# Kernel tuning notes

Hardware: AMD Instinct MI355X
Metric: run time of the kernel (lower is better)

## Reference

```python
import jax, jax.numpy as jnp
import numpy as np

WP, WF, OUT_W = 10, 10, 110  # past/future window, fixed alpha width from source


def setup_inputs() -> dict:
    key = jax.random.key(0)
    k1, k2, k3 = jax.random.split(key, 3)
    B, L, D = 4096, 110, 200
    node_features = jax.random.normal(k1, (B, L, D), dtype=jnp.float32)
    text_len_tensor = jax.random.randint(k2, (B,), 1, L + 1)  # valid lengths in [1, L]
    var = 2.0 / (D + D)  # init std from source
    weight = jax.random.normal(k3, (D, D), dtype=jnp.float32) * var
    return {"node_features": node_features, "text_len_tensor": text_len_tensor, "weight": weight}


def reference(node_features, text_len_tensor, weight):
    B, L, D = node_features.shape
    # att_matrix[b,k] = W @ x[b,k]
    att = jnp.einsum('de,bke->bkd', weight, node_features)
    # score[b,j,k] = att[b,k] . x[b,j]  (query token j attends over window of k)
    scores = jnp.einsum('bkd,bjd->bjk', att, node_features)
    j = jnp.arange(L)[None, :, None]
    k = jnp.arange(L)[None, None, :]
    lens = text_len_tensor[:, None, None]
    s = jnp.maximum(j - WP, 0)
    e = jnp.minimum(j + WF, lens - 1)
    mask = (k >= s) & (k <= e) & (j < lens)
    probs = jax.nn.softmax(jnp.where(mask, scores, jnp.asarray(-1e9, scores.dtype)), axis=-1)
    probs = jnp.where(mask, probs, jnp.asarray(0.0, probs.dtype))
    # scatter into fixed-width alpha [L, 110] per batch, rows j>=len stay zero
    out = jnp.zeros((B, L, OUT_W), node_features.dtype).at[:, :, :L].set(probs)
    return out
```

## Files before the change

kernel.cpp:

```cpp
#include <hip/hip_runtime.h>
#include <stdint.h>

typedef short short8 __attribute__((ext_vector_type(8)));
typedef float floatx4 __attribute__((ext_vector_type(4)));
typedef int int4v __attribute__((ext_vector_type(4)));

#define NB 4096
#define LL 110
#define DD 200
#define WPP 10
#define WFF 10
#define OUTW 110

#define MTI 7
#define NTI 13
#define KCH 7
#define LDSTR 232

static __device__ __forceinline__ short f32_bf16_rn(float f) {
    uint32_t u = __float_as_uint(f);
    u += 0x7FFFu + ((u >> 16) & 1u);
    return (short)(u >> 16);
}

__global__ void EdgeAtt_wswz(const float* __restrict__ W, short* __restrict__ wswz) {
    const int nt = blockIdx.x / KCH;
    const int kc = blockIdx.x % KCH;
    const int l  = threadIdx.x;
    const int e  = nt * 16 + (l & 15);
    const int db = kc * 32 + (l >> 4) * 8;
    short8 v;
#pragma unroll
    for (int i = 0; i < 8; ++i) {
        int d = db + i;
        float x = (d < DD && e < DD) ? W[d * DD + e] : 0.0f;
        v[i] = f32_bf16_rn(x);
    }
    *(short8*)(wswz + ((size_t)(kc * NTI + nt) * 64 + l) * 8) = v;
}

__global__ __launch_bounds__(512) void EdgeAtt_fused(
    const float* __restrict__ nf, const int* __restrict__ lens,
    const short* __restrict__ wswz, float* __restrict__ out)
{
    __shared__ short nfb[112 * LDSTR];
    __shared__ short ylds[112 * LDSTR];
    const int b    = blockIdx.x;
    const int tid  = threadIdx.x;
    const int lane = tid & 63;
    const int wave = tid >> 6;
    const int len  = lens[b];

    {
        int4v z = {0, 0, 0, 0};
        for (int i = tid; i < (112 * LDSTR) / 8; i += 512) {
            ((int4v*)nfb)[i]  = z;
            ((int4v*)ylds)[i] = z;
        }
    }
    __syncthreads();

    {
        const float4* src = (const float4*)(nf + (size_t)b * LL * DD);
        for (int idx = tid; idx < (LL * DD) / 4; idx += 512) {
            float4 v = src[idx];
            int j = (idx * 4) / DD;
            int d = (idx * 4) % DD;
            uint32_t lo = ((uint32_t)(uint16_t)f32_bf16_rn(v.y) << 16) | (uint16_t)f32_bf16_rn(v.x);
            uint32_t hi = ((uint32_t)(uint16_t)f32_bf16_rn(v.w) << 16) | (uint16_t)f32_bf16_rn(v.z);
            uint32_t* dst = (uint32_t*)&nfb[j * LDSTR + d];
            dst[0] = lo;
            dst[1] = hi;
        }
    }
    __syncthreads();

    {
        const int wm   = wave >> 2;
        const int wn   = wave & 3;
        const int arow = lane & 15;
        const int acol = (lane >> 4) * 8;
        for (int nt = wn; nt < NTI; nt += 4) {
            short8 bf[KCH];
#pragma unroll
            for (int kc = 0; kc < KCH; ++kc)
                bf[kc] = *(const short8*)(wswz + ((size_t)(kc * NTI + nt) * 64 + lane) * 8);
            for (int mt = wm; mt < MTI; mt += 2) {
                floatx4 acc = {0.f, 0.f, 0.f, 0.f};
                const short* abase = &nfb[(mt * 16 + arow) * LDSTR + acol];
#pragma unroll
                for (int kc = 0; kc < KCH; ++kc) {
                    short8 a = *(const short8*)(abase + kc * 32);
                    acc = __builtin_amdgcn_mfma_f32_16x16x32_bf16(a, bf[kc], acc, 0, 0, 0);
                }
                const int col = nt * 16 + (lane & 15);
                const int rb  = mt * 16 + (lane >> 4) * 4;
#pragma unroll
                for (int i = 0; i < 4; ++i)
                    ylds[(rb + i) * LDSTR + col] = f32_bf16_rn(acc[i]);
            }
        }
    }
    __syncthreads();

    if (wave < 7) {
        const int jt = wave;
        int kts[3];
#pragma unroll
        for (int t = 0; t < 3; ++t) {
            int kt = jt - 1 + t;
            kt = kt < 0 ? 0 : kt;
            kt = kt > (MTI - 1) ? (MTI - 1) : kt;
            kts[t] = kt;
        }
        floatx4 acc[3] = {{0,0,0,0},{0,0,0,0},{0,0,0,0}};
        const int r16  = lane & 15;
        const int acol = (lane >> 4) * 8;
#pragma unroll
        for (int kc = 0; kc < KCH; ++kc) {
            short8 a = *(const short8*)&ylds[(jt * 16 + r16) * LDSTR + kc * 32 + acol];
#pragma unroll
            for (int t = 0; t < 3; ++t) {
                short8 bb = *(const short8*)&nfb[(kts[t] * 16 + r16) * LDSTR + kc * 32 + acol];
                acc[t] = __builtin_amdgcn_mfma_f32_16x16x32_bf16(a, bb, acc[t], 0, 0, 0);
            }
        }
        const int g  = lane >> 4;
        const int kl = lane & 15;
#pragma unroll
        for (int i = 0; i < 4; ++i) {
            const int j = jt * 16 + g * 4 + i;
            if (j >= LL) continue;
            const bool jv = (j < len);
            int slo = j - WPP; slo = slo < 0 ? 0 : slo;
            int shi = j + WFF; { int lm = len - 1; shi = shi > lm ? lm : shi; }
            float sv[3], ev[3];
            bool  kv[3];
            float m = -1e30f;
#pragma unroll
            for (int t = 0; t < 3; ++t) {
                int k = kts[t] * 16 + kl;
                bool tv = (t == 0) || (kts[t] != kts[t - 1]);
                kv[t] = jv && tv && (k >= slo) && (k <= shi);
                sv[t] = acc[t][i];
                if (kv[t]) m = fmaxf(m, sv[t]);
            }
#pragma unroll
            for (int o = 1; o < 16; o <<= 1) m = fmaxf(m, __shfl_xor(m, o, 64));
            float sum = 0.f;
#pragma unroll
            for (int t = 0; t < 3; ++t) {
                ev[t] = kv[t] ? __expf(sv[t] - m) : 0.f;
                sum += ev[t];
            }
#pragma unroll
            for (int o = 1; o < 16; o <<= 1) sum += __shfl_xor(sum, o, 64);
            const float inv = jv ? (1.0f / sum) : 0.0f;
            float* orow = out + ((size_t)b * LL + j) * OUTW;
#pragma unroll
            for (int kt = 0; kt < 7; ++kt) {
                int k = kt * 16 + kl;
                if (k >= OUTW) continue;
                float v = 0.0f;
                if      (kts[0] == kt) v = ev[0] * inv;
                else if (kts[1] == kt) v = ev[1] * inv;
                else if (kts[2] == kt) v = ev[2] * inv;
                orow[k] = v;
            }
        }
    }
}

extern "C" void kernel_launch(void* const* d_in, const int* in_sizes, int n_in,
                              void* d_out, int out_size, void* d_ws, size_t ws_size,
                              hipStream_t stream) {
    const float* nf   = (const float*)d_in[0];
    const int*   lens = (const int*)d_in[1];
    const float* W    = (const float*)d_in[2];
    short* wswz = (short*)d_ws;
    float* out  = (float*)d_out;

    hipLaunchKernelGGL(EdgeAtt_wswz, dim3(KCH * NTI), dim3(64), 0, stream, W, wswz);
    hipLaunchKernelGGL(EdgeAtt_fused, dim3(NB), dim3(512), 0, stream, nf, lens, wswz, out);
}
```

Baseline: 678.3 us.

## Split each batch across two blocks by query-row halves to raise occupancy

Each batch item is now handled by two blocks. Each block covers a range of query rows (0-63 or 64-109) and loads only the key rows its band window needs (80 or 64 rows). This shrinks LDS per block from two 112-row buffers so more blocks fit per CU, and launch bounds request 4 blocks. The cost is redundant loading and conversion of the overlapping rows (48-79), plus a restructured W-projection GEMM where each wave keeps its A fragments in registers and streams W from global/L2.

```diff
diff --git a/kernel.cpp b/kernel.cpp
--- a/kernel.cpp
+++ b/kernel.cpp
@@ -12,10 +12,12 @@
 #define WFF 10
 #define OUTW 110
 
-#define MTI 7
 #define NTI 13
 #define KCH 7
 #define LDSTR 232
+
+#define NFROWS 80
+#define YROWS 64
 
 static __device__ __forceinline__ short f32_bf16_rn(float f) {
     uint32_t u = __float_as_uint(f);
@@ -39,78 +41,84 @@
     *(short8*)(wswz + ((size_t)(kc * NTI + nt) * 64 + l) * 8) = v;
 }
 
-__global__ __launch_bounds__(512) void EdgeAtt_fused(
+__global__ __launch_bounds__(512, 4) void EdgeAtt_fused(
     const float* __restrict__ nf, const int* __restrict__ lens,
     const short* __restrict__ wswz, float* __restrict__ out)
 {
-    __shared__ short nfb[112 * LDSTR];
-    __shared__ short ylds[112 * LDSTR];
-    const int b    = blockIdx.x;
+    __shared__ short nfb[NFROWS * LDSTR];
+    __shared__ short ylds[YROWS * LDSTR];
+    const int b    = blockIdx.x >> 1;
+    const int h    = blockIdx.x & 1;
     const int tid  = threadIdx.x;
     const int lane = tid & 63;
     const int wave = tid >> 6;
     const int len  = lens[b];
 
+    const int base  = h ? 48 : 0;
+    const int nrows = h ? 64 : 80;
+    const int j0    = h ? 64 : 0;
+    const int njt   = h ? 3  : 4;
+
     {
         int4v z = {0, 0, 0, 0};
-        for (int i = tid; i < (112 * LDSTR) / 8; i += 512) {
-            ((int4v*)nfb)[i]  = z;
-            ((int4v*)ylds)[i] = z;
-        }
+        for (int i = tid; i < (NFROWS * LDSTR) / 8; i += 512) ((int4v*)nfb)[i] = z;
+        for (int i = tid; i < (YROWS * LDSTR) / 8; i += 512)  ((int4v*)ylds)[i] = z;
     }
     __syncthreads();
 
     {
         const float4* src = (const float4*)(nf + (size_t)b * LL * DD);
-        for (int idx = tid; idx < (LL * DD) / 4; idx += 512) {
-            float4 v = src[idx];
-            int j = (idx * 4) / DD;
-            int d = (idx * 4) % DD;
-            uint32_t lo = ((uint32_t)(uint16_t)f32_bf16_rn(v.y) << 16) | (uint16_t)f32_bf16_rn(v.x);
-            uint32_t hi = ((uint32_t)(uint16_t)f32_bf16_rn(v.w) << 16) | (uint16_t)f32_bf16_rn(v.z);
-            uint32_t* dst = (uint32_t*)&nfb[j * LDSTR + d];
-            dst[0] = lo;
-            dst[1] = hi;
-        }
-    }
-    __syncthreads();
-
-    {
-        const int wm   = wave >> 2;
-        const int wn   = wave & 3;
-        const int arow = lane & 15;
-        const int acol = (lane >> 4) * 8;
-        for (int nt = wn; nt < NTI; nt += 4) {
-            short8 bf[KCH];
-#pragma unroll
-            for (int kc = 0; kc < KCH; ++kc)
-                bf[kc] = *(const short8*)(wswz + ((size_t)(kc * NTI + nt) * 64 + lane) * 8);
-            for (int mt = wm; mt < MTI; mt += 2) {
-                floatx4 acc = {0.f, 0.f, 0.f, 0.f};
-                const short* abase = &nfb[(mt * 16 + arow) * LDSTR + acol];
-#pragma unroll
-                for (int kc = 0; kc < KCH; ++kc) {
-                    short8 a = *(const short8*)(abase + kc * 32);
-                    acc = __builtin_amdgcn_mfma_f32_16x16x32_bf16(a, bf[kc], acc, 0, 0, 0);
-                }
-                const int col = nt * 16 + (lane & 15);
-                const int rb  = mt * 16 + (lane >> 4) * 4;
-#pragma unroll
-                for (int i = 0; i < 4; ++i)
-                    ylds[(rb + i) * LDSTR + col] = f32_bf16_rn(acc[i]);
+        const int nf4 = nrows * (DD / 4);
+        for (int idx = tid; idx < nf4; idx += 512) {
+            int rl = idx / (DD / 4);
+            int d  = (idx % (DD / 4)) * 4;
+            int rg = base + rl;
+            if (rg < LL) {
+                float4 v = src[rg * (DD / 4) + d / 4];
+                uint32_t lo = ((uint32_t)(uint16_t)f32_bf16_rn(v.y) << 16) | (uint16_t)f32_bf16_rn(v.x);
+                uint32_t hi = ((uint32_t)(uint16_t)f32_bf16_rn(v.w) << 16) | (uint16_t)f32_bf16_rn(v.z);
+                uint32_t* dst = (uint32_t*)&nfb[rl * LDSTR + d];
+                dst[0] = lo;
+                dst[1] = hi;
             }
         }
     }
     __syncthreads();
 
-    if (wave < 7) {
-        const int jt = wave;
+    if (wave < 2 * njt) {
+        const int mt_l = wave % njt;
+        const int wn   = wave / njt;
+        const int rowA = (j0 - base) + mt_l * 16 + (lane & 15);
+        const int acol = (lane >> 4) * 8;
+        short8 af[KCH];
+#pragma unroll
+        for (int kc = 0; kc < KCH; ++kc)
+            af[kc] = *(const short8*)&nfb[rowA * LDSTR + kc * 32 + acol];
+        for (int nt = wn; nt < NTI; nt += 2) {
+            floatx4 acc = {0.f, 0.f, 0.f, 0.f};
+#pragma unroll
+            for (int kc = 0; kc < KCH; ++kc) {
+                short8 bf = *(const short8*)(wswz + ((size_t)(kc * NTI + nt) * 64 + lane) * 8);
+                acc = __builtin_amdgcn_mfma_f32_16x16x32_bf16(af[kc], bf, acc, 0, 0, 0);
+            }
+            const int col = nt * 16 + (lane & 15);
+            const int rb  = mt_l * 16 + (lane >> 4) * 4;
+#pragma unroll
+            for (int i = 0; i < 4; ++i)
+                ylds[(rb + i) * LDSTR + col] = f32_bf16_rn(acc[i]);
+        }
+    }
+    __syncthreads();
+
+    if (wave < njt) {
+        const int jt_g = j0 / 16 + wave;
+        const int ktb  = base / 16;
         int kts[3];
 #pragma unroll
         for (int t = 0; t < 3; ++t) {
-            int kt = jt - 1 + t;
+            int kt = jt_g - 1 + t;
             kt = kt < 0 ? 0 : kt;
-            kt = kt > (MTI - 1) ? (MTI - 1) : kt;
+            kt = kt > 6 ? 6 : kt;
             kts[t] = kt;
         }
         floatx4 acc[3] = {{0,0,0,0},{0,0,0,0},{0,0,0,0}};
@@ -118,10 +126,10 @@
         const int acol = (lane >> 4) * 8;
 #pragma unroll
         for (int kc = 0; kc < KCH; ++kc) {
-            short8 a = *(const short8*)&ylds[(jt * 16 + r16) * LDSTR + kc * 32 + acol];
+            short8 a = *(const short8*)&ylds[(wave * 16 + r16) * LDSTR + kc * 32 + acol];
 #pragma unroll
             for (int t = 0; t < 3; ++t) {
-                short8 bb = *(const short8*)&nfb[(kts[t] * 16 + r16) * LDSTR + kc * 32 + acol];
+                short8 bb = *(const short8*)&nfb[((kts[t] - ktb) * 16 + r16) * LDSTR + kc * 32 + acol];
                 acc[t] = __builtin_amdgcn_mfma_f32_16x16x32_bf16(a, bb, acc[t], 0, 0, 0);
             }
         }
@@ -129,7 +137,7 @@
         const int kl = lane & 15;
 #pragma unroll
         for (int i = 0; i < 4; ++i) {
-            const int j = jt * 16 + g * 4 + i;
+            const int j = jt_g * 16 + g * 4 + i;
             if (j >= LL) continue;
             const bool jv = (j < len);
             int slo = j - WPP; slo = slo < 0 ? 0 : slo;
@@ -181,5 +189,5 @@
     float* out  = (float*)d_out;
 
     hipLaunchKernelGGL(EdgeAtt_wswz, dim3(KCH * NTI), dim3(64), 0, stream, W, wswz);
-    hipLaunchKernelGGL(EdgeAtt_fused, dim3(NB), dim3(512), 0, stream, nf, lens, wswz, out);
+    hipLaunchKernelGGL(EdgeAtt_fused, dim3(NB * 2), dim3(512), 0, stream, nf, lens, wswz, out);
 }
```

Result: faster. 664.7 us (-2.0%).

## Restructure to one wave per 16-row query tile with register-resident intermediate

Applied to the files above, without the earlier changes.

Replaces the per-batch block with per-wave units (batch, query tile). Each wave loads its node-feature fragments straight from global memory into registers and computes the transposed W·x product with W held in LDS. It then reshuffles the bf16 accumulators across lanes to form the A operand for the score MFMA, so no intermediate goes through LDS. This removes the LDS zeroing, the staging and the block-wide barriers, and raises occupancy. In exchange, the neighbouring key tiles are re-read from global memory (L2), the 13 accumulators increase register pressure, and every block copies W into LDS.

```diff
diff --git a/kernel.cpp b/kernel.cpp
--- a/kernel.cpp
+++ b/kernel.cpp
@@ -4,6 +4,7 @@
 typedef short short8 __attribute__((ext_vector_type(8)));
 typedef float floatx4 __attribute__((ext_vector_type(4)));
 typedef int int4v __attribute__((ext_vector_type(4)));
+typedef unsigned int uint;
 
 #define NB 4096
 #define LL 110
@@ -12,15 +13,16 @@
 #define WFF 10
 #define OUTW 110
 
-#define MTI 7
 #define NTI 13
 #define KCH 7
-#define LDSTR 232
 
 static __device__ __forceinline__ short f32_bf16_rn(float f) {
     uint32_t u = __float_as_uint(f);
     u += 0x7FFFu + ((u >> 16) & 1u);
     return (short)(u >> 16);
+}
+static __device__ __forceinline__ uint pack2bf(float lo, float hi) {
+    return ((uint)(unsigned short)f32_bf16_rn(hi) << 16) | (unsigned short)f32_bf16_rn(lo);
 }
 
 __global__ void EdgeAtt_wswz(const float* __restrict__ W, short* __restrict__ wswz) {
@@ -39,134 +41,145 @@
     *(short8*)(wswz + ((size_t)(kc * NTI + nt) * 64 + l) * 8) = v;
 }
 
-__global__ __launch_bounds__(512) void EdgeAtt_fused(
+static __device__ __forceinline__ short8 ld_nf_frag(const float* __restrict__ nf,
+                                                    int b, int rt, int kc, int g, int r) {
+    short8 s = {0, 0, 0, 0, 0, 0, 0, 0};
+    const int cb = kc * 32 + g * 8;
+    if (cb < DD) {
+        int row = rt * 16 + r;
+        row = row > (LL - 1) ? (LL - 1) : row;
+        const float* p = nf + ((size_t)b * LL + row) * DD + cb;
+        float4 a = *(const float4*)p;
+        float4 c = *(const float4*)(p + 4);
+        s[0] = f32_bf16_rn(a.x); s[1] = f32_bf16_rn(a.y);
+        s[2] = f32_bf16_rn(a.z); s[3] = f32_bf16_rn(a.w);
+        s[4] = f32_bf16_rn(c.x); s[5] = f32_bf16_rn(c.y);
+        s[6] = f32_bf16_rn(c.z); s[7] = f32_bf16_rn(c.w);
+    }
+    return s;
+}
+
+__global__ __launch_bounds__(1024) void EdgeAtt_fused(
     const float* __restrict__ nf, const int* __restrict__ lens,
     const short* __restrict__ wswz, float* __restrict__ out)
 {
-    __shared__ short nfb[112 * LDSTR];
-    __shared__ short ylds[112 * LDSTR];
-    const int b    = blockIdx.x;
-    const int tid  = threadIdx.x;
+    __shared__ short wlds[KCH * NTI * 64 * 8];
+    const int tid = threadIdx.x;
+
+    for (int idx = tid; idx < KCH * NTI * 64; idx += 1024)
+        ((short8*)wlds)[idx] = ((const short8*)wswz)[idx];
+    __syncthreads();
+
     const int lane = tid & 63;
     const int wave = tid >> 6;
+    const int unit = blockIdx.x * 16 + wave;
+    const int b    = unit / 7;
+    const int jt   = unit % 7;
+    const int g    = lane >> 4;
+    const int r    = lane & 15;
     const int len  = lens[b];
 
-    {
-        int4v z = {0, 0, 0, 0};
-        for (int i = tid; i < (112 * LDSTR) / 8; i += 512) {
-            ((int4v*)nfb)[i]  = z;
-            ((int4v*)ylds)[i] = z;
+    short8 jf[KCH];
+#pragma unroll
+    for (int kc = 0; kc < KCH; ++kc)
+        jf[kc] = ld_nf_frag(nf, b, jt, kc, g, r);
+
+    floatx4 acc[NTI];
+#pragma unroll
+    for (int nt = 0; nt < NTI; ++nt) acc[nt] = (floatx4){0.f, 0.f, 0.f, 0.f};
+#pragma unroll
+    for (int kc = 0; kc < KCH; ++kc) {
+#pragma unroll
+        for (int nt = 0; nt < NTI; ++nt) {
+            short8 wf = *(const short8*)&wlds[((kc * NTI + nt) * 64 + lane) * 8];
+            acc[nt] = __builtin_amdgcn_mfma_f32_16x16x32_bf16(wf, jf[kc], acc[nt], 0, 0, 0);
         }
     }
-    __syncthreads();
 
-    {
-        const float4* src = (const float4*)(nf + (size_t)b * LL * DD);
-        for (int idx = tid; idx < (LL * DD) / 4; idx += 512) {
-            float4 v = src[idx];
-            int j = (idx * 4) / DD;
-            int d = (idx * 4) % DD;
-            uint32_t lo = ((uint32_t)(uint16_t)f32_bf16_rn(v.y) << 16) | (uint16_t)f32_bf16_rn(v.x);
-            uint32_t hi = ((uint32_t)(uint16_t)f32_bf16_rn(v.w) << 16) | (uint16_t)f32_bf16_rn(v.z);
-            uint32_t* dst = (uint32_t*)&nfb[j * LDSTR + d];
-            dst[0] = lo;
-            dst[1] = hi;
+    int kts[3];
+#pragma unroll
+    for (int t = 0; t < 3; ++t) {
+        int kt = jt - 1 + t;
+        kt = kt < 0 ? 0 : kt;
+        kt = kt > 6 ? 6 : kt;
+        kts[t] = kt;
+    }
+    floatx4 acc2[3] = {{0,0,0,0},{0,0,0,0},{0,0,0,0}};
+    const int src0 = (((2 * g) & 3) << 4) | r;
+    const int src1 = (((2 * g + 1) & 3) << 4) | r;
+    const bool lohalf = (g < 2);
+#pragma unroll
+    for (int kc = 0; kc < KCH; ++kc) {
+        const int nlo = 2 * kc;
+        const int nhi = (kc < 6) ? (2 * kc + 1) : 12;
+        uint plo0 = pack2bf(acc[nlo][0], acc[nlo][1]);
+        uint plo1 = pack2bf(acc[nlo][2], acc[nlo][3]);
+        uint phi0 = pack2bf(acc[nhi][0], acc[nhi][1]);
+        uint phi1 = pack2bf(acc[nhi][2], acc[nhi][3]);
+        uint l0 = (uint)__shfl((int)plo0, src0);
+        uint l1 = (uint)__shfl((int)plo1, src0);
+        uint l2 = (uint)__shfl((int)plo0, src1);
+        uint l3 = (uint)__shfl((int)plo1, src1);
+        uint h0 = (uint)__shfl((int)phi0, src0);
+        uint h1 = (uint)__shfl((int)phi1, src0);
+        uint h2 = (uint)__shfl((int)phi0, src1);
+        uint h3 = (uint)__shfl((int)phi1, src1);
+        const bool pad = (kc == 6) && (g >= 2);
+        uint d0 = pad ? 0u : (lohalf ? l0 : h0);
+        uint d1 = pad ? 0u : (lohalf ? l1 : h1);
+        uint d2 = pad ? 0u : (lohalf ? l2 : h2);
+        uint d3 = pad ? 0u : (lohalf ? l3 : h3);
+        int4v a2i; a2i[0] = (int)d0; a2i[1] = (int)d1; a2i[2] = (int)d2; a2i[3] = (int)d3;
+        short8 a2 = *(short8*)&a2i;
+#pragma unroll
+        for (int t = 0; t < 3; ++t) {
+            short8 bf;
+            if (kts[t] == jt) bf = jf[kc];
+            else              bf = ld_nf_frag(nf, b, kts[t], kc, g, r);
+            acc2[t] = __builtin_amdgcn_mfma_f32_16x16x32_bf16(a2, bf, acc2[t], 0, 0, 0);
         }
     }
-    __syncthreads();
 
-    {
-        const int wm   = wave >> 2;
-        const int wn   = wave & 3;
-        const int arow = lane & 15;
-        const int acol = (lane >> 4) * 8;
-        for (int nt = wn; nt < NTI; nt += 4) {
-            short8 bf[KCH];
+    const int kl = r;
 #pragma unroll
-            for (int kc = 0; kc < KCH; ++kc)
-                bf[kc] = *(const short8*)(wswz + ((size_t)(kc * NTI + nt) * 64 + lane) * 8);
-            for (int mt = wm; mt < MTI; mt += 2) {
-                floatx4 acc = {0.f, 0.f, 0.f, 0.f};
-                const short* abase = &nfb[(mt * 16 + arow) * LDSTR + acol];
-#pragma unroll
-                for (int kc = 0; kc < KCH; ++kc) {
-                    short8 a = *(const short8*)(abase + kc * 32);
-                    acc = __builtin_amdgcn_mfma_f32_16x16x32_bf16(a, bf[kc], acc, 0, 0, 0);
-                }
-                const int col = nt * 16 + (lane & 15);
-                const int rb  = mt * 16 + (lane >> 4) * 4;
-#pragma unroll
-                for (int i = 0; i < 4; ++i)
-                    ylds[(rb + i) * LDSTR + col] = f32_bf16_rn(acc[i]);
-            }
-        }
-    }
-    __syncthreads();
-
-    if (wave < 7) {
-        const int jt = wave;
-        int kts[3];
+    for (int i = 0; i < 4; ++i) {
+        const int j = jt * 16 + g * 4 + i;
+        if (j >= LL) continue;
+        const bool jv = (j < len);
+        int slo = j - WPP; slo = slo < 0 ? 0 : slo;
+        int shi = j + WFF; { int lm = len - 1; shi = shi > lm ? lm : shi; }
+        float sv[3], ev[3];
+        bool  kv[3];
+        float m = -1e30f;
 #pragma unroll
         for (int t = 0; t < 3; ++t) {
-            int kt = jt - 1 + t;
-            kt = kt < 0 ? 0 : kt;
-            kt = kt > (MTI - 1) ? (MTI - 1) : kt;
-            kts[t] = kt;
+            int k = kts[t] * 16 + kl;
+            bool tv = (t == 0) || (kts[t] != kts[t - 1]);
+            kv[t] = jv && tv && (k >= slo) && (k <= shi);
+            sv[t] = acc2[t][i];
+            if (kv[t]) m = fmaxf(m, sv[t]);
         }
-        floatx4 acc[3] = {{0,0,0,0},{0,0,0,0},{0,0,0,0}};
-        const int r16  = lane & 15;
-        const int acol = (lane >> 4) * 8;
 #pragma unroll
-        for (int kc = 0; kc < KCH; ++kc) {
-            short8 a = *(const short8*)&ylds[(jt * 16 + r16) * LDSTR + kc * 32 + acol];
+        for (int o = 1; o < 16; o <<= 1) m = fmaxf(m, __shfl_xor(m, o, 64));
+        float sum = 0.f;
 #pragma unroll
-            for (int t = 0; t < 3; ++t) {
-                short8 bb = *(const short8*)&nfb[(kts[t] * 16 + r16) * LDSTR + kc * 32 + acol];
-                acc[t] = __builtin_amdgcn_mfma_f32_16x16x32_bf16(a, bb, acc[t], 0, 0, 0);
-            }
+        for (int t = 0; t < 3; ++t) {
+            ev[t] = kv[t] ? __expf(sv[t] - m) : 0.f;
+            sum += ev[t];
         }
-        const int g  = lane >> 4;
-        const int kl = lane & 15;
 #pragma unroll
-        for (int i = 0; i < 4; ++i) {
-            const int j = jt * 16 + g * 4 + i;
-            if (j >= LL) continue;
-            const bool jv = (j < len);
-            int slo = j - WPP; slo = slo < 0 ? 0 : slo;
-            int shi = j + WFF; { int lm = len - 1; shi = shi > lm ? lm : shi; }
-            float sv[3], ev[3];
-            bool  kv[3];
-            float m = -1e30f;
+        for (int o = 1; o < 16; o <<= 1) sum += __shfl_xor(sum, o, 64);
+        const float inv = jv ? (1.0f / sum) : 0.0f;
+        float* orow = out + ((size_t)b * LL + j) * OUTW;
 #pragma unroll
-            for (int t = 0; t < 3; ++t) {
-                int k = kts[t] * 16 + kl;
-                bool tv = (t == 0) || (kts[t] != kts[t - 1]);
-                kv[t] = jv && tv && (k >= slo) && (k <= shi);
-                sv[t] = acc[t][i];
-                if (kv[t]) m = fmaxf(m, sv[t]);
-            }
-#pragma unroll
-            for (int o = 1; o < 16; o <<= 1) m = fmaxf(m, __shfl_xor(m, o, 64));
-            float sum = 0.f;
-#pragma unroll
-            for (int t = 0; t < 3; ++t) {
-                ev[t] = kv[t] ? __expf(sv[t] - m) : 0.f;
-                sum += ev[t];
-            }
-#pragma unroll
-            for (int o = 1; o < 16; o <<= 1) sum += __shfl_xor(sum, o, 64);
-            const float inv = jv ? (1.0f / sum) : 0.0f;
-            float* orow = out + ((size_t)b * LL + j) * OUTW;
-#pragma unroll
-            for (int kt = 0; kt < 7; ++kt) {
-                int k = kt * 16 + kl;
-                if (k >= OUTW) continue;
-                float v = 0.0f;
-                if      (kts[0] == kt) v = ev[0] * inv;
-                else if (kts[1] == kt) v = ev[1] * inv;
-                else if (kts[2] == kt) v = ev[2] * inv;
-                orow[k] = v;
-            }
+        for (int kt = 0; kt < 7; ++kt) {
+            int k = kt * 16 + kl;
+            if (k >= OUTW) continue;
+            float v = 0.0f;
+            if      (kts[0] == kt) v = ev[0] * inv;
+            else if (kts[1] == kt) v = ev[1] * inv;
+            else if (kts[2] == kt) v = ev[2] * inv;
+            orow[k] = v;
         }
     }
 }
@@ -181,5 +194,5 @@
     float* out  = (float*)d_out;
 
     hipLaunchKernelGGL(EdgeAtt_wswz, dim3(KCH * NTI), dim3(64), 0, stream, W, wswz);
-    hipLaunchKernelGGL(EdgeAtt_fused, dim3(NB), dim3(512), 0, stream, nf, lens, wswz, out);
+    hipLaunchKernelGGL(EdgeAtt_fused, dim3(1792), dim3(1024), 0, stream, nf, lens, wswz, out);
 }
```

After: 623.4 us. -8.1%, faster.
